# Performance work log

Measured on AMD Instinct MI355X. Metric: run time of the kernel, lower is better.

Reference implementation:

```python
import jax, jax.numpy as jnp
import numpy as np

WINDOW_LEN = 256
HOP_LEN = 128
LOG_EPS = 1e-8


def setup_inputs() -> dict:
    key = jax.random.key(0)
    # (batch=64, eeg_channels=23, n_samples=30720)  ~ 2 min @ 256 Hz
    signal = jax.random.normal(key, (64, 23, 30720), dtype=jnp.float32)
    return {"signal": signal}


def _hanning(m):
    # matches np.hanning: symmetric Hann window of length m
    n = jnp.arange(m, dtype=jnp.float32)
    return 0.5 - 0.5 * jnp.cos(2.0 * jnp.pi * n / (m - 1))


def reference(signal):
    wl, hop = WINDOW_LEN, HOP_LEN
    window = _hanning(wl)
    n_windows = (signal.shape[-1] - wl) // hop + 1  # static
    # gather indices for all frames: (n_windows, wl)
    idx = jnp.arange(n_windows)[:, None] * hop + jnp.arange(wl)[None, :]
    frames = signal[..., idx] * window          # (..., n_windows, wl)
    spec = jnp.fft.rfft(frames, n=wl, axis=-1)  # (..., n_windows, wl//2+1) complex
    # log_scale=True branch of the module
    return jnp.log(jnp.abs(spec) + LOG_EPS) * 10.0
```

## Files before the change

kernel.cpp:

```cpp
#include <hip/hip_runtime.h>
#include <math.h>

#define WL     256
#define HOP    128
#define NW     239
#define NBINS  129
#define NSAMP  30720
#define NROWS  (64*23)

__global__ __launch_bounds__(64) void stft_kernel(const float* __restrict__ sig,
                                                  float* __restrict__ out) {
    const int t   = threadIdx.x;
    const int bid = blockIdx.x;
    const int row = bid / NW;
    const int w   = bid - row * NW;
    const float* __restrict__ src = sig + (size_t)row * NSAMP + (size_t)w * HOP;

    __shared__ float re[128], im[128];
    __shared__ float twc[132], tws[132];

    for (int k = t; k <= 128; k += 64) {
        float s, c;
        sincospif((float)k * (1.0f / 128.0f), &s, &c);
        twc[k] = c;
        tws[k] = -s;
    }

    #pragma unroll
    for (int q = 0; q < 4; ++q) {
        int sidx = t + 64 * q;
        float v = src[sidx];
        float wnd = 0.5f - 0.5f * cospif(2.0f * (float)sidx * (1.0f / 255.0f));
        v *= wnd;
        if (sidx & 1) im[sidx >> 1] = v;
        else          re[sidx >> 1] = v;
    }
    __syncthreads();

    #pragma unroll
    for (int lm = 7; lm >= 1; --lm) {
        const int half = 1 << (lm - 1);
        const int j    = t & (half - 1);
        const int i0   = ((t >> (lm - 1)) << lm) + j;
        const int i1   = i0 + half;
        const int tw   = j << (8 - lm);
        float ar = re[i0], ai = im[i0];
        float br = re[i1], bi = im[i1];
        float c = twc[tw], s = tws[tw];
        float tr = ar - br, ti = ai - bi;
        re[i0] = ar + br;
        im[i0] = ai + bi;
        re[i1] = tr * c - ti * s;
        im[i1] = tr * s + ti * c;
        __syncthreads();
    }

    float* __restrict__ o = out + (size_t)bid * NBINS;
    #pragma unroll
    for (int q = 0; q < 2; ++q) {
        int k  = t + 64 * q;
        int pk = (int)(__brev((unsigned)(k & 127)) >> 25);
        int pm = (int)(__brev((unsigned)((128 - k) & 127)) >> 25);
        float zkr = re[pk], zki = im[pk];
        float zmr = re[pm], zmi = im[pm];
        float er  = 0.5f * (zkr + zmr);
        float ei  = 0.5f * (zki - zmi);
        float orr = 0.5f * (zki + zmi);
        float oi  = -0.5f * (zkr - zmr);
        float c = twc[k], s = tws[k];
        float Xr = er + c * orr - s * oi;
        float Xi = ei + c * oi + s * orr;
        float mag = sqrtf(Xr * Xr + Xi * Xi);
        o[k] = logf(mag + 1e-8f) * 10.0f;
    }
    if (t == 0) {
        float Xr = re[0] - im[0];
        o[128] = logf(fabsf(Xr) + 1e-8f) * 10.0f;
    }
}

extern "C" void kernel_launch(void* const* d_in, const int* in_sizes, int n_in,
                              void* d_out, int out_size, void* d_ws, size_t ws_size,
                              hipStream_t stream) {
    const float* sig = (const float*)d_in[0];
    float* out = (float*)d_out;
    (void)in_sizes; (void)n_in; (void)out_size; (void)d_ws; (void)ws_size;
    const int nblocks = NROWS * NW;
    stft_kernel<<<dim3(nblocks), dim3(64), 0, stream>>>(sig, out);
}
```

Before: 442.0 us.

## Run the 128-point FFT in registers with wavefront shuffles instead of LDS

```diff
diff --git a/kernel.cpp b/kernel.cpp
--- a/kernel.cpp
+++ b/kernel.cpp
@@ -10,72 +10,101 @@
 
 __global__ __launch_bounds__(64) void stft_kernel(const float* __restrict__ sig,
                                                   float* __restrict__ out) {
-    const int t   = threadIdx.x;
+    const int l   = threadIdx.x;
     const int bid = blockIdx.x;
     const int row = bid / NW;
     const int w   = bid - row * NW;
     const float* __restrict__ src = sig + (size_t)row * NSAMP + (size_t)w * HOP;
 
-    __shared__ float re[128], im[128];
-    __shared__ float twc[132], tws[132];
+    __shared__ __align__(8) float zre[128];
+    __shared__ __align__(8) float zim[128];
 
-    for (int k = t; k <= 128; k += 64) {
+    float2 xa = *reinterpret_cast<const float2*>(src + 2 * l);
+    float2 xb = *reinterpret_cast<const float2*>(src + 2 * l + 128);
+    float w0 = 0.5f - 0.5f * cospif((float)(4 * l)       * (1.0f / 255.0f));
+    float w1 = 0.5f - 0.5f * cospif((float)(4 * l + 2)   * (1.0f / 255.0f));
+    float w2 = 0.5f - 0.5f * cospif((float)(4 * l + 256) * (1.0f / 255.0f));
+    float w3 = 0.5f - 0.5f * cospif((float)(4 * l + 258) * (1.0f / 255.0f));
+    float v0r = xa.x * w0, v0i = xa.y * w1;
+    float v1r = xb.x * w2, v1i = xb.y * w3;
+
+    {
         float s, c;
-        sincospif((float)k * (1.0f / 128.0f), &s, &c);
-        twc[k] = c;
-        tws[k] = -s;
+        sincospif((float)l * (1.0f / 64.0f), &s, &c);
+        float tr = v0r - v1r, ti = v0i - v1i;
+        v0r += v1r; v0i += v1i;
+        v1r = tr * c + ti * s;
+        v1i = ti * c - tr * s;
     }
 
     #pragma unroll
-    for (int q = 0; q < 4; ++q) {
-        int sidx = t + 64 * q;
-        float v = src[sidx];
-        float wnd = 0.5f - 0.5f * cospif(2.0f * (float)sidx * (1.0f / 255.0f));
-        v *= wnd;
-        if (sidx & 1) im[sidx >> 1] = v;
-        else          re[sidx >> 1] = v;
+    for (int m = 32; m >= 4; m >>= 1) {
+        float s, c;
+        sincospif((float)(l & (m - 1)) * (1.0f / (float)m), &s, &c);
+        const bool up = (l & m) != 0;
+        float p0r = __shfl_xor(v0r, m), p0i = __shfl_xor(v0i, m);
+        float p1r = __shfl_xor(v1r, m), p1i = __shfl_xor(v1i, m);
+        float dr = p0r - v0r, di = p0i - v0i;
+        float wr = dr * c + di * s, wi = di * c - dr * s;
+        v0r = up ? wr : (v0r + p0r);
+        v0i = up ? wi : (v0i + p0i);
+        dr = p1r - v1r; di = p1i - v1i;
+        wr = dr * c + di * s; wi = di * c - dr * s;
+        v1r = up ? wr : (v1r + p1r);
+        v1i = up ? wi : (v1i + p1i);
     }
+
+    {
+        const bool up = (l & 2) != 0;
+        const bool j1 = (l & 1) != 0;
+        float p0r = __shfl_xor(v0r, 2), p0i = __shfl_xor(v0i, 2);
+        float p1r = __shfl_xor(v1r, 2), p1i = __shfl_xor(v1i, 2);
+        float dr = p0r - v0r, di = p0i - v0i;
+        float wr = j1 ? di : dr, wi = j1 ? -dr : di;
+        v0r = up ? wr : (v0r + p0r);
+        v0i = up ? wi : (v0i + p0i);
+        dr = p1r - v1r; di = p1i - v1i;
+        wr = j1 ? di : dr; wi = j1 ? -dr : di;
+        v1r = up ? wr : (v1r + p1r);
+        v1i = up ? wi : (v1i + p1i);
+    }
+
+    {
+        const bool up = (l & 1) != 0;
+        float p0r = __shfl_xor(v0r, 1), p0i = __shfl_xor(v0i, 1);
+        float p1r = __shfl_xor(v1r, 1), p1i = __shfl_xor(v1i, 1);
+        v0r = up ? (p0r - v0r) : (v0r + p0r);
+        v0i = up ? (p0i - v0i) : (v0i + p0i);
+        v1r = up ? (p1r - v1r) : (v1r + p1r);
+        v1i = up ? (p1i - v1i) : (v1i + p1i);
+    }
+
+    const int pn = (int)(__brev((unsigned)l) >> 26);
+    reinterpret_cast<float2*>(zre)[pn] = make_float2(v0r, v1r);
+    reinterpret_cast<float2*>(zim)[pn] = make_float2(v0i, v1i);
     __syncthreads();
-
-    #pragma unroll
-    for (int lm = 7; lm >= 1; --lm) {
-        const int half = 1 << (lm - 1);
-        const int j    = t & (half - 1);
-        const int i0   = ((t >> (lm - 1)) << lm) + j;
-        const int i1   = i0 + half;
-        const int tw   = j << (8 - lm);
-        float ar = re[i0], ai = im[i0];
-        float br = re[i1], bi = im[i1];
-        float c = twc[tw], s = tws[tw];
-        float tr = ar - br, ti = ai - bi;
-        re[i0] = ar + br;
-        im[i0] = ai + bi;
-        re[i1] = tr * c - ti * s;
-        im[i1] = tr * s + ti * c;
-        __syncthreads();
-    }
 
     float* __restrict__ o = out + (size_t)bid * NBINS;
     #pragma unroll
     for (int q = 0; q < 2; ++q) {
-        int k  = t + 64 * q;
-        int pk = (int)(__brev((unsigned)(k & 127)) >> 25);
-        int pm = (int)(__brev((unsigned)((128 - k) & 127)) >> 25);
-        float zkr = re[pk], zki = im[pk];
-        float zmr = re[pm], zmi = im[pm];
+        int k  = l + 64 * q;
+        int km = (128 - k) & 127;
+        float zkr = zre[k],  zki = zim[k];
+        float zmr = zre[km], zmi = zim[km];
         float er  = 0.5f * (zkr + zmr);
         float ei  = 0.5f * (zki - zmi);
         float orr = 0.5f * (zki + zmi);
         float oi  = -0.5f * (zkr - zmr);
-        float c = twc[k], s = tws[k];
-        float Xr = er + c * orr - s * oi;
-        float Xi = ei + c * oi + s * orr;
+        float s, c;
+        sincospif((float)k * (1.0f / 128.0f), &s, &c);
+        float Xr = er + c * orr + s * oi;
+        float Xi = ei + c * oi - s * orr;
         float mag = sqrtf(Xr * Xr + Xi * Xi);
-        o[k] = logf(mag + 1e-8f) * 10.0f;
+        o[k] = __log2f(mag + 1e-8f) * 6.931471805599453f;
     }
-    if (t == 0) {
-        float Xr = re[0] - im[0];
-        o[128] = logf(fabsf(Xr) + 1e-8f) * 10.0f;
+    if (l == 0) {
+        float Xr = zre[0] - zim[0];
+        o[128] = __log2f(fabsf(Xr) + 1e-8f) * 6.931471805599453f;
     }
 }
 
```

New measurement: 463.2 us. 1.05x slower.
